# Kernel optimization log

Hardware: AMD Instinct MI355X
Metric: run time of the kernel (lower is better)

The kernel has to match this reference:

```python
import jax, jax.numpy as jnp
import numpy as np

B, S, D_MODEL, D_FF, E, K = 4, 2048, 1024, 4096, 8, 2
CAP_FACTOR = 1.0


def setup_inputs() -> dict:
    key = jax.random.key(0)
    ks = jax.random.split(key, 6)
    std = 0.02
    return {
        "x": jax.random.normal(ks[0], (B, S, D_MODEL), jnp.float32),
        "router_w": jax.random.normal(ks[1], (E, D_MODEL), jnp.float32) * std,  # Linear(d_model,E,bias=False) weight
        "w1": jax.random.normal(ks[2], (E, D_MODEL, D_FF), jnp.float32) * std,
        "b1": jnp.zeros((E, D_FF), jnp.float32),
        "w2": jax.random.normal(ks[3], (E, D_FF, D_MODEL), jnp.float32) * std,
        "b2": jnp.zeros((E, D_MODEL), jnp.float32),
    }


def reference(x, router_w, w1, b1, w2, b2):
    b, s, d = x.shape
    T = b * s
    e = router_w.shape[0]
    capacity = int(CAP_FACTOR * T / e)  # static
    xf = x.reshape(T, d)

    # --- routing ---
    logits = xf @ router_w.T                       # [T,E]
    probs = jax.nn.softmax(logits, axis=-1)
    vals, idx = jax.lax.top_k(probs, K)            # [T,K] values / expert ids
    vals = vals / vals.sum(-1, keepdims=True)

    # dense gate matrix [T,E]; top_k experts are distinct so this is a scatter of K weights per token
    ar = jnp.arange(T)
    gates = jnp.zeros((T, e), x.dtype).at[ar[:, None], idx].add(vals)

    # --- load-balancing loss ---
    counts = jnp.zeros((e,), jnp.float32).at[idx.reshape(-1)].add(1.0)
    ideal = T * K / e
    lb_loss = jnp.sum((counts - ideal) ** 2) / (T ** 2)

    # --- capacity-limited dispatch (first `capacity` tokens in token order per expert) ---
    mask = gates > 0                                               # [T,E]
    order = jnp.argsort(jnp.logical_not(mask), axis=0)[:capacity]  # stable: assigned tokens first, ascending token id -> [cap,E]
    valid = jnp.take_along_axis(mask, order, axis=0)               # [cap,E] token actually assigned & within capacity
    idx_ec = order.T                                               # [E,cap]

    # --- grouped expert MLP ---
    xg = xf[idx_ec]                                                # [E,cap,D]
    h = jax.nn.gelu(jnp.einsum('ecd,edf->ecf', xg, w1) + b1[:, None, :], approximate=False)
    y = jnp.einsum('ecf,efd->ecd', h, w2) + b2[:, None, :]         # [E,cap,D]

    # --- combine (scatter-add with routing weights; dropped/invalid slots get weight 0) ---
    wt = gates[idx_ec, jnp.arange(e)[:, None]] * valid.T           # [E,cap]
    out = jnp.zeros((T, d), x.dtype).at[idx_ec.reshape(-1)].add((y * wt[..., None]).reshape(-1, d))
    return out.reshape(b, s, d), lb_loss
```

## Files before the change

kernel.cpp:

```cpp
#include <hip/hip_runtime.h>
#include <hip/hip_bf16.h>

#define T_TOK 8192
#define DMODEL 1024
#define DFF 4096
#define NEXP 8
#define CAP 1024

typedef __attribute__((ext_vector_type(8))) __bf16 bf16x8;
typedef __attribute__((ext_vector_type(4))) float f32x4;

__device__ __forceinline__ unsigned short f2bf(float f) {
  union { float f; unsigned int u; } v;
  v.f = f;
  return (unsigned short)((v.u + 0x7fffu + ((v.u >> 16) & 1u)) >> 16);
}

__device__ __forceinline__ float bfbits2f(unsigned int lo16) {
  union { unsigned int u; float f; } v; v.u = lo16 << 16; return v.f;
}

__device__ __forceinline__ float fast_gelu(float v) {
  float x = fabsf(v) * 0.70710678118654752440f;
  float t = __builtin_amdgcn_rcpf(1.0f + 0.3275911f * x);
  float poly = t * (0.254829592f + t * (-0.284496736f + t * (1.421413741f +
               t * (-1.453152027f + t * 1.061405429f))));
  float er = 1.0f - poly * __expf(-x * x);
  float s = (v >= 0.0f) ? er : -er;
  return 0.5f * v * (1.0f + s);
}

__device__ __forceinline__ void load_lds16(const unsigned short* g, unsigned short* l) {
  __builtin_amdgcn_global_load_lds((const __attribute__((address_space(1))) void*)g,
                                   (__attribute__((address_space(3))) void*)l,
                                   16, 0, 0);
}

__global__ void k_router(const float* __restrict__ x, const float* __restrict__ rw,
                         unsigned short* __restrict__ xb,
                         int* __restrict__ tk_idx, float* __restrict__ tk_w,
                         int* __restrict__ tinv) {
  if (threadIdx.x < 8) tinv[blockIdx.x * 8 + threadIdx.x] = -1;
  int wv = threadIdx.x >> 6, lane = threadIdx.x & 63;
  int t = blockIdx.x * 4 + wv;
  const float4* xr = (const float4*)(x + (size_t)t * DMODEL);
  uint2* xbw = (uint2*)(xb + (size_t)t * DMODEL);
  float acc[NEXP];
#pragma unroll
  for (int e = 0; e < NEXP; ++e) acc[e] = 0.f;
#pragma unroll
  for (int j = 0; j < DMODEL / 256; ++j) {
    float4 v = xr[j * 64 + lane];
#pragma unroll
    for (int e = 0; e < NEXP; ++e) {
      float4 w = ((const float4*)(rw + e * DMODEL))[j * 64 + lane];
      acc[e] += v.x * w.x + v.y * w.y + v.z * w.z + v.w * w.w;
    }
    uint2 p;
    p.x = (unsigned int)f2bf(v.x) | ((unsigned int)f2bf(v.y) << 16);
    p.y = (unsigned int)f2bf(v.z) | ((unsigned int)f2bf(v.w) << 16);
    xbw[j * 64 + lane] = p;
  }
#pragma unroll
  for (int e = 0; e < NEXP; ++e)
    for (int off = 32; off; off >>= 1) acc[e] += __shfl_xor(acc[e], off);
  if (lane == 0) {
    int i0 = 0;
    for (int e = 1; e < NEXP; ++e) if (acc[e] > acc[i0]) i0 = e;
    int i1 = (i0 == 0) ? 1 : 0;
    for (int e = 0; e < NEXP; ++e) if (e != i0 && acc[e] > acc[i1]) i1 = e;
    float ex = expf(acc[i1] - acc[i0]);
    float w0 = 1.f / (1.f + ex);
    float w1 = ex / (1.f + ex);
    tk_idx[2 * t] = i0; tk_idx[2 * t + 1] = i1;
    tk_w[2 * t] = w0;  tk_w[2 * t + 1] = w1;
  }
}

__global__ void k_transpose_cvt(const float* __restrict__ src, unsigned short* __restrict__ dst,
                                int Kd, int Nd) {
  __shared__ unsigned short tile[64][73];
  int e = blockIdx.z;
  size_t k0 = (size_t)blockIdx.y * 64, n0 = (size_t)blockIdx.x * 64;
  int tid = threadIdx.x;
  const float* sb = src + (size_t)e * Kd * Nd;
  int r = tid >> 4, cg = (tid & 15) * 4;
  for (int rr = 0; rr < 4; ++rr) {
    int row = r + rr * 16;
    float4 v = *(const float4*)(sb + (k0 + row) * Nd + n0 + cg);
    tile[row][cg + 0] = f2bf(v.x);
    tile[row][cg + 1] = f2bf(v.y);
    tile[row][cg + 2] = f2bf(v.z);
    tile[row][cg + 3] = f2bf(v.w);
  }
  __syncthreads();
  unsigned short* db = dst + (size_t)e * Nd * Kd;
  int rn = tid >> 3, kg = (tid & 7) * 8;
  for (int rr = 0; rr < 2; ++rr) {
    int nrow = rn + rr * 32;
    union { unsigned short h[8]; uint4 v; } o;
#pragma unroll
    for (int j = 0; j < 8; ++j) o.h[j] = tile[kg + j][nrow];
    *(uint4*)(db + (n0 + nrow) * Kd + k0 + kg) = o.v;
  }
}

__global__ void k_scan(const int* __restrict__ tk_idx, const float* __restrict__ tk_w,
                       int* __restrict__ etok, float* __restrict__ egate,
                       int* __restrict__ tinv, int* __restrict__ counts) {
  __shared__ int wavecnt[8][16];
  __shared__ int waveoff[8][16];
  int e = blockIdx.x;
  int tid = threadIdx.x, lane = tid & 63, wv = tid >> 6;
  for (int i = tid; i < CAP; i += 1024) etok[e * CAP + i] = 0;
  unsigned long long lt = (1ULL << lane) - 1ULL;
  int pos[8], wh[8];
  bool mine[8];
#pragma unroll
  for (int c = 0; c < 8; ++c) {
    int t = c * 1024 + tid;
    int e0 = tk_idx[2 * t], e1 = tk_idx[2 * t + 1];
    bool is0 = (e0 == e), is1 = (e1 == e);
    mine[c] = is0 || is1;
    wh[c] = is1 ? 1 : 0;
    unsigned long long bal = __ballot(mine[c]);
    pos[c] = __popcll(bal & lt);
    if (lane == 0) wavecnt[c][wv] = __popcll(bal);
  }
  __syncthreads();
  if (tid == 0) {
    int s = 0;
    for (int c = 0; c < 8; ++c)
      for (int w = 0; w < 16; ++w) { waveoff[c][w] = s; s += wavecnt[c][w]; }
    counts[e] = s;
  }
  __syncthreads();
#pragma unroll
  for (int c = 0; c < 8; ++c) {
    if (mine[c]) {
      int t = c * 1024 + tid;
      int r = waveoff[c][wv] + pos[c];
      if (r < CAP) {
        etok[e * CAP + r] = t;
        egate[e * CAP + r] = tk_w[2 * t + wh[c]];
        tinv[2 * t + wh[c]] = e * CAP + r;
      }
    }
  }
}

__global__ __launch_bounds__(256) void k_gemm1(
    const unsigned short* __restrict__ xb, const unsigned short* __restrict__ w1t,
    const float* __restrict__ b1, const int* __restrict__ etok,
    unsigned short* __restrict__ H) {
  __shared__ __align__(16) unsigned short smem[24576];
  int tid = threadIdx.x;
  int lane = tid & 63, wv = tid >> 6;
  int bid = blockIdx.x;
  int e = bid >> 8;
  int b = bid & 255;
  int nl = b & 7, m = (b >> 3) & 7, nh = b >> 6;
  int m0 = m * 128, n0 = (nh * 8 + nl) * 128;

  const unsigned short* gA[2];
  const unsigned short* gB[2];
  int wb[2];
#pragma unroll
  for (int s = 0; s < 2; ++s) {
    int i = s * 256 + tid;
    int row = i >> 2;
    int q = (i & 3) ^ ((i >> 3) & 3);
    int tok = etok[e * CAP + m0 + row];
    gA[s] = xb + (size_t)tok * DMODEL + q * 8;
    gB[s] = w1t + ((size_t)e * DFF + n0 + row) * DMODEL + q * 8;
    wb[s] = (s * 256 + wv * 64) * 8;
  }

  f32x4 zero = {0.f, 0.f, 0.f, 0.f};
  f32x4 acc[4][4];
#pragma unroll
  for (int mi = 0; mi < 4; ++mi)
#pragma unroll
    for (int ni = 0; ni < 4; ++ni) acc[mi][ni] = zero;

  int wm = (wv >> 1) * 64, wn = (wv & 1) * 64;
  int fr = lane & 15, quad = lane >> 4;
  int cs = (quad ^ ((fr >> 1) & 3)) * 8;
  int aoff = (wm + fr) * 32 + cs;
  int boff = (wn + fr) * 32 + cs;

#pragma unroll
  for (int s = 0; s < 2; ++s) {
    load_lds16(gA[s], smem + wb[s]);
    load_lds16(gB[s], smem + 4096 + wb[s]);
  }
#pragma unroll
  for (int s = 0; s < 2; ++s) {
    load_lds16(gA[s] + 32, smem + 8192 + wb[s]);
    load_lds16(gB[s] + 32, smem + 8192 + 4096 + wb[s]);
  }

  const int NT = DMODEL / 32;
  int cur = 0, stg = 16384;
  for (int t = 0; t < NT; ++t) {
    if (t < NT - 1) asm volatile("s_waitcnt vmcnt(4)" ::: "memory");
    else            asm volatile("s_waitcnt vmcnt(0)" ::: "memory");
    __builtin_amdgcn_s_barrier();
    asm volatile("" ::: "memory");
    if (t + 2 < NT) {
      int kp = (t + 2) * 32;
#pragma unroll
      for (int s = 0; s < 2; ++s) {
        load_lds16(gA[s] + kp, smem + stg + wb[s]);
        load_lds16(gB[s] + kp, smem + stg + 4096 + wb[s]);
      }
      stg += 8192; if (stg == 24576) stg = 0;
    }
    const unsigned short* Ab = smem + cur;
    const unsigned short* Bb = Ab + 4096;
    bf16x8 av[4], bv[4];
#pragma unroll
    for (int mi = 0; mi < 4; ++mi) av[mi] = *(const bf16x8*)(Ab + aoff + mi * 512);
#pragma unroll
    for (int ni = 0; ni < 4; ++ni) bv[ni] = *(const bf16x8*)(Bb + boff + ni * 512);
#pragma unroll
    for (int mi = 0; mi < 4; ++mi)
#pragma unroll
      for (int ni = 0; ni < 4; ++ni)
        acc[mi][ni] = __builtin_amdgcn_mfma_f32_16x16x32_bf16(bv[ni], av[mi], acc[mi][ni], 0, 0, 0);
    cur += 8192; if (cur == 24576) cur = 0;
  }
  __syncthreads();

  unsigned short* EP = smem + wv * 1536;
#pragma unroll
  for (int ni = 0; ni < 4; ++ni) {
    float4 b4 = *(const float4*)(b1 + e * DFF + n0 + wn + ni * 16 + quad * 4);
#pragma unroll
    for (int mi = 0; mi < 4; ++mi) {
      float v0 = fast_gelu(acc[mi][ni][0] + b4.x);
      float v1 = fast_gelu(acc[mi][ni][1] + b4.y);
      float v2 = fast_gelu(acc[mi][ni][2] + b4.z);
      float v3 = fast_gelu(acc[mi][ni][3] + b4.w);
      uint2 p;
      p.x = (unsigned int)f2bf(v0) | ((unsigned int)f2bf(v1) << 16);
      p.y = (unsigned int)f2bf(v2) | ((unsigned int)f2bf(v3) << 16);
      *(uint2*)(EP + (mi * 16 + fr) * 24 + quad * 4) = p;
    }
#pragma unroll
    for (int t = 0; t < 2; ++t) {
      int row = t * 32 + (lane >> 1), chunk = lane & 1;
      uint4 v = *(const uint4*)(EP + row * 24 + chunk * 8);
      *(uint4*)(H + ((size_t)e * CAP + m0 + wm + row) * DFF + n0 + wn + ni * 16 + chunk * 8) = v;
    }
  }
}

__global__ __launch_bounds__(256) void k_gemm2(
    const unsigned short* __restrict__ H, const unsigned short* __restrict__ w2t,
    const float* __restrict__ b2, unsigned short* __restrict__ Y) {
  __shared__ __align__(16) unsigned short smem[24576];
  int tid = threadIdx.x;
  int lane = tid & 63, wv = tid >> 6;
  int bid = blockIdx.x;
  int e = bid & 7;
  int r = bid >> 3;
  int n0 = (r & 7) * 128;
  int m0 = (r >> 3) * 128;

  const unsigned short* gA[2];
  const unsigned short* gB[2];
  int wb[2];
#pragma unroll
  for (int s = 0; s < 2; ++s) {
    int i = s * 256 + tid;
    int row = i >> 2;
    int q = (i & 3) ^ ((i >> 3) & 3);
    gA[s] = H + ((size_t)e * CAP + m0 + row) * DFF + q * 8;
    gB[s] = w2t + ((size_t)e * DMODEL + n0 + row) * DFF + q * 8;
    wb[s] = (s * 256 + wv * 64) * 8;
  }

  f32x4 zero = {0.f, 0.f, 0.f, 0.f};
  f32x4 acc[4][4];
#pragma unroll
  for (int mi = 0; mi < 4; ++mi)
#pragma unroll
    for (int ni = 0; ni < 4; ++ni) acc[mi][ni] = zero;

  int wm = (wv >> 1) * 64, wn = (wv & 1) * 64;
  int fr = lane & 15, quad = lane >> 4;
  int cs = (quad ^ ((fr >> 1) & 3)) * 8;
  int aoff = (wm + fr) * 32 + cs;
  int boff = (wn + fr) * 32 + cs;

#pragma unroll
  for (int s = 0; s < 2; ++s) {
    load_lds16(gA[s], smem + wb[s]);
    load_lds16(gB[s], smem + 4096 + wb[s]);
  }
#pragma unroll
  for (int s = 0; s < 2; ++s) {
    load_lds16(gA[s] + 32, smem + 8192 + wb[s]);
    load_lds16(gB[s] + 32, smem + 8192 + 4096 + wb[s]);
  }

  const int NT = DFF / 32;
  int cur = 0, stg = 16384;
  for (int t = 0; t < NT; ++t) {
    if (t < NT - 1) asm volatile("s_waitcnt vmcnt(4)" ::: "memory");
    else            asm volatile("s_waitcnt vmcnt(0)" ::: "memory");
    __builtin_amdgcn_s_barrier();
    asm volatile("" ::: "memory");
    if (t + 2 < NT) {
      int kp = (t + 2) * 32;
#pragma unroll
      for (int s = 0; s < 2; ++s) {
        load_lds16(gA[s] + kp, smem + stg + wb[s]);
        load_lds16(gB[s] + kp, smem + stg + 4096 + wb[s]);
      }
      stg += 8192; if (stg == 24576) stg = 0;
    }
    const unsigned short* Ab = smem + cur;
    const unsigned short* Bb = Ab + 4096;
    bf16x8 av[4], bv[4];
#pragma unroll
    for (int mi = 0; mi < 4; ++mi) av[mi] = *(const bf16x8*)(Ab + aoff + mi * 512);
#pragma unroll
    for (int ni = 0; ni < 4; ++ni) bv[ni] = *(const bf16x8*)(Bb + boff + ni * 512);
#pragma unroll
    for (int mi = 0; mi < 4; ++mi)
#pragma unroll
      for (int ni = 0; ni < 4; ++ni)
        acc[mi][ni] = __builtin_amdgcn_mfma_f32_16x16x32_bf16(bv[ni], av[mi], acc[mi][ni], 0, 0, 0);
    cur += 8192; if (cur == 24576) cur = 0;
  }
  __syncthreads();

  unsigned short* EP = smem + wv * 1536;
#pragma unroll
  for (int ni = 0; ni < 4; ++ni) {
    float4 b4 = *(const float4*)(b2 + e * DMODEL + n0 + wn + ni * 16 + quad * 4);
#pragma unroll
    for (int mi = 0; mi < 4; ++mi) {
      uint2 p;
      p.x = (unsigned int)f2bf(acc[mi][ni][0] + b4.x) |
            ((unsigned int)f2bf(acc[mi][ni][1] + b4.y) << 16);
      p.y = (unsigned int)f2bf(acc[mi][ni][2] + b4.z) |
            ((unsigned int)f2bf(acc[mi][ni][3] + b4.w) << 16);
      *(uint2*)(EP + (mi * 16 + fr) * 24 + quad * 4) = p;
    }
#pragma unroll
    for (int t = 0; t < 2; ++t) {
      int row = t * 32 + (lane >> 1), chunk = lane & 1;
      uint4 v = *(const uint4*)(EP + row * 24 + chunk * 8);
      *(uint4*)(Y + ((size_t)e * CAP + m0 + wm + row) * DMODEL + n0 + wn + ni * 16 + chunk * 8) = v;
    }
  }
}

__global__ void k_combine(const unsigned short* __restrict__ Y,
                          const float* __restrict__ egate,
                          const int* __restrict__ tinv,
                          const int* __restrict__ counts,
                          float* __restrict__ out, float* __restrict__ loss_out) {
  int t = blockIdx.x, tid = threadIdx.x;
  int s0 = tinv[2 * t], s1 = tinv[2 * t + 1];
  int d0 = tid * 4;
  float a0 = 0.f, a1 = 0.f, a2 = 0.f, a3 = 0.f;
  if (s0 >= 0) {
    float g = egate[s0];
    uint2 v = *(const uint2*)(Y + (size_t)s0 * DMODEL + d0);
    a0 += g * bfbits2f(v.x & 0xffff); a1 += g * bfbits2f(v.x >> 16);
    a2 += g * bfbits2f(v.y & 0xffff); a3 += g * bfbits2f(v.y >> 16);
  }
  if (s1 >= 0) {
    float g = egate[s1];
    uint2 v = *(const uint2*)(Y + (size_t)s1 * DMODEL + d0);
    a0 += g * bfbits2f(v.x & 0xffff); a1 += g * bfbits2f(v.x >> 16);
    a2 += g * bfbits2f(v.y & 0xffff); a3 += g * bfbits2f(v.y >> 16);
  }
  float4 o = {a0, a1, a2, a3};
  *(float4*)(out + (size_t)t * DMODEL + d0) = o;
  if (t == 0 && tid == 0) {
    float loss = 0.f;
    for (int e = 0; e < NEXP; ++e) {
      float d = (float)counts[e] - 2048.0f;
      loss += d * d;
    }
    loss_out[0] = loss / (8192.0f * 8192.0f);
  }
}

extern "C" void kernel_launch(void* const* d_in, const int* in_sizes, int n_in,
                              void* d_out, int out_size, void* d_ws, size_t ws_size,
                              hipStream_t stream) {
  (void)in_sizes; (void)n_in; (void)ws_size; (void)out_size;
  const float* x  = (const float*)d_in[0];
  const float* rw = (const float*)d_in[1];
  const float* w1 = (const float*)d_in[2];
  const float* b1 = (const float*)d_in[3];
  const float* w2 = (const float*)d_in[4];
  const float* b2 = (const float*)d_in[5];
  float* out = (float*)d_out;

  char* ws = (char*)d_ws;
  const size_t XB_BYTES = (size_t)T_TOK * DMODEL * 2;
  const size_t WT_BYTES = (size_t)NEXP * DFF * DMODEL * 2;
  const size_t H_BYTES  = (size_t)NEXP * CAP * DFF * 2;
  unsigned short* xb = (unsigned short*)ws;
  unsigned short* Yb = xb;
  unsigned short* wT = (unsigned short*)(ws + XB_BYTES);
  unsigned short* Hb = (unsigned short*)(ws + XB_BYTES + WT_BYTES);
  char* small = ws + XB_BYTES + WT_BYTES + H_BYTES;
  int*   etok   = (int*)small;
  float* egate  = (float*)(small + NEXP * CAP * 4);
  int*   tkidx  = (int*)(small + 2 * NEXP * CAP * 4);
  float* tkw    = (float*)(small + 2 * NEXP * CAP * 4 + T_TOK * 2 * 4);
  int*   tinv   = (int*)(small + 2 * NEXP * CAP * 4 + 2 * T_TOK * 2 * 4);
  int*   counts = (int*)(small + 2 * NEXP * CAP * 4 + 3 * T_TOK * 2 * 4);

  k_router<<<T_TOK / 4, 256, 0, stream>>>(x, rw, xb, tkidx, tkw, tinv);
  k_scan<<<NEXP, 1024, 0, stream>>>(tkidx, tkw, etok, egate, tinv, counts);
  k_transpose_cvt<<<dim3(DFF / 64, DMODEL / 64, NEXP), 256, 0, stream>>>(w1, wT, DMODEL, DFF);
  k_gemm1<<<NEXP * 256, 256, 0, stream>>>(xb, wT, b1, etok, Hb);
  k_transpose_cvt<<<dim3(DMODEL / 64, DFF / 64, NEXP), 256, 0, stream>>>(w2, wT, DFF, DMODEL);
  k_gemm2<<<NEXP * 64, 256, 0, stream>>>(Hb, wT, b2, Yb);
  k_combine<<<T_TOK, 256, 0, stream>>>(Yb, egate, tinv, counts, out,
                                       out + (size_t)T_TOK * DMODEL);
}
```

Measured before the change: 544.7 us.

## Fuse combine into gemm2 epilogue with atomic scatter-add and smaller tiles

Removes the separate combine kernel and the bf16 Y buffer: gemm2 now applies bias and gate and atomically adds results directly into the fp32 output, which the router kernel zero-initialises. The gemm2 tile shrinks from 128x128 to 64x128 with double buffering instead of triple, doubling the block count so the grid fills more CUs. The atomics add contention and nondeterministic summation order, and the simpler pipeline with a full barrier per k-step may expose more memory latency.

```diff
diff --git a/kernel.cpp b/kernel.cpp
--- a/kernel.cpp
+++ b/kernel.cpp
@@ -14,10 +14,6 @@
   union { float f; unsigned int u; } v;
   v.f = f;
   return (unsigned short)((v.u + 0x7fffu + ((v.u >> 16) & 1u)) >> 16);
-}
-
-__device__ __forceinline__ float bfbits2f(unsigned int lo16) {
-  union { unsigned int u; float f; } v; v.u = lo16 << 16; return v.f;
 }
 
 __device__ __forceinline__ float fast_gelu(float v) {
@@ -39,10 +35,15 @@
 __global__ void k_router(const float* __restrict__ x, const float* __restrict__ rw,
                          unsigned short* __restrict__ xb,
                          int* __restrict__ tk_idx, float* __restrict__ tk_w,
-                         int* __restrict__ tinv) {
-  if (threadIdx.x < 8) tinv[blockIdx.x * 8 + threadIdx.x] = -1;
+                         float* __restrict__ out) {
   int wv = threadIdx.x >> 6, lane = threadIdx.x & 63;
   int t = blockIdx.x * 4 + wv;
+  {
+    float4 z = {0.f, 0.f, 0.f, 0.f};
+    float4* orow = (float4*)(out + (size_t)t * DMODEL);
+#pragma unroll
+    for (int j = 0; j < 4; ++j) orow[j * 64 + lane] = z;
+  }
   const float4* xr = (const float4*)(x + (size_t)t * DMODEL);
   uint2* xbw = (uint2*)(xb + (size_t)t * DMODEL);
   float acc[NEXP];
@@ -107,12 +108,15 @@
 
 __global__ void k_scan(const int* __restrict__ tk_idx, const float* __restrict__ tk_w,
                        int* __restrict__ etok, float* __restrict__ egate,
-                       int* __restrict__ tinv, int* __restrict__ counts) {
+                       int* __restrict__ counts) {
   __shared__ int wavecnt[8][16];
   __shared__ int waveoff[8][16];
   int e = blockIdx.x;
   int tid = threadIdx.x, lane = tid & 63, wv = tid >> 6;
-  for (int i = tid; i < CAP; i += 1024) etok[e * CAP + i] = 0;
+  for (int i = tid; i < CAP; i += 1024) {
+    etok[e * CAP + i] = 0;
+    egate[e * CAP + i] = 0.f;
+  }
   unsigned long long lt = (1ULL << lane) - 1ULL;
   int pos[8], wh[8];
   bool mine[8];
@@ -143,7 +147,6 @@
       if (r < CAP) {
         etok[e * CAP + r] = t;
         egate[e * CAP + r] = tk_w[2 * t + wh[c]];
-        tinv[2 * t + wh[c]] = e * CAP + r;
       }
     }
   }
@@ -258,137 +261,99 @@
 
 __global__ __launch_bounds__(256) void k_gemm2(
     const unsigned short* __restrict__ H, const unsigned short* __restrict__ w2t,
-    const float* __restrict__ b2, unsigned short* __restrict__ Y) {
-  __shared__ __align__(16) unsigned short smem[24576];
+    const float* __restrict__ b2, const int* __restrict__ etok,
+    const float* __restrict__ egate, const int* __restrict__ counts,
+    float* __restrict__ out, float* __restrict__ loss_out) {
+  __shared__ __align__(16) unsigned short smem[12288];
   int tid = threadIdx.x;
   int lane = tid & 63, wv = tid >> 6;
   int bid = blockIdx.x;
+  if (bid == 0 && tid == 0) {
+    float loss = 0.f;
+    for (int ee = 0; ee < NEXP; ++ee) {
+      float d = (float)counts[ee] - 2048.0f;
+      loss += d * d;
+    }
+    loss_out[0] = loss / (8192.0f * 8192.0f);
+  }
   int e = bid & 7;
   int r = bid >> 3;
   int n0 = (r & 7) * 128;
-  int m0 = (r >> 3) * 128;
-
-  const unsigned short* gA[2];
-  const unsigned short* gB[2];
-  int wb[2];
-#pragma unroll
-  for (int s = 0; s < 2; ++s) {
+  int m0 = (r >> 3) * 64;
+
+  const unsigned short* g[3];
+  int wb[3];
+#pragma unroll
+  for (int s = 0; s < 3; ++s) {
     int i = s * 256 + tid;
-    int row = i >> 2;
-    int q = (i & 3) ^ ((i >> 3) & 3);
-    gA[s] = H + ((size_t)e * CAP + m0 + row) * DFF + q * 8;
-    gB[s] = w2t + ((size_t)e * DMODEL + n0 + row) * DFF + q * 8;
-    wb[s] = (s * 256 + wv * 64) * 8;
+    wb[s] = i * 8;
+    if (s == 0) {
+      int row = i >> 2;
+      int q = (i & 3) ^ ((i >> 3) & 3);
+      g[s] = H + ((size_t)e * CAP + m0 + row) * DFF + q * 8;
+    } else {
+      int ii = i - 256;
+      int row = ii >> 2;
+      int q = (ii & 3) ^ ((ii >> 3) & 3);
+      g[s] = w2t + ((size_t)e * DMODEL + n0 + row) * DFF + q * 8;
+    }
   }
 
   f32x4 zero = {0.f, 0.f, 0.f, 0.f};
-  f32x4 acc[4][4];
+  f32x4 acc[4][2];
 #pragma unroll
   for (int mi = 0; mi < 4; ++mi)
 #pragma unroll
-    for (int ni = 0; ni < 4; ++ni) acc[mi][ni] = zero;
-
-  int wm = (wv >> 1) * 64, wn = (wv & 1) * 64;
+    for (int ni = 0; ni < 2; ++ni) acc[mi][ni] = zero;
+
+  int wn = wv * 32;
   int fr = lane & 15, quad = lane >> 4;
   int cs = (quad ^ ((fr >> 1) & 3)) * 8;
-  int aoff = (wm + fr) * 32 + cs;
+  int aoff = fr * 32 + cs;
   int boff = (wn + fr) * 32 + cs;
 
 #pragma unroll
-  for (int s = 0; s < 2; ++s) {
-    load_lds16(gA[s], smem + wb[s]);
-    load_lds16(gB[s], smem + 4096 + wb[s]);
-  }
-#pragma unroll
-  for (int s = 0; s < 2; ++s) {
-    load_lds16(gA[s] + 32, smem + 8192 + wb[s]);
-    load_lds16(gB[s] + 32, smem + 8192 + 4096 + wb[s]);
-  }
-
-  const int NT = DFF / 32;
-  int cur = 0, stg = 16384;
-  for (int t = 0; t < NT; ++t) {
-    if (t < NT - 1) asm volatile("s_waitcnt vmcnt(4)" ::: "memory");
-    else            asm volatile("s_waitcnt vmcnt(0)" ::: "memory");
-    __builtin_amdgcn_s_barrier();
-    asm volatile("" ::: "memory");
-    if (t + 2 < NT) {
-      int kp = (t + 2) * 32;
-#pragma unroll
-      for (int s = 0; s < 2; ++s) {
-        load_lds16(gA[s] + kp, smem + stg + wb[s]);
-        load_lds16(gB[s] + kp, smem + stg + 4096 + wb[s]);
+  for (int s = 0; s < 3; ++s) load_lds16(g[s], smem + wb[s]);
+  int buf = 0;
+  for (int k0 = 32; k0 <= DFF; k0 += 32) {
+    __syncthreads();
+    int nbuf = buf ^ 6144;
+    if (k0 < DFF) {
+#pragma unroll
+      for (int s = 0; s < 3; ++s) load_lds16(g[s] + k0, smem + nbuf + wb[s]);
+    }
+    const unsigned short* Ab = smem + buf;
+    const unsigned short* Bb = Ab + 2048;
+    bf16x8 av[4], bv[2];
+#pragma unroll
+    for (int mi = 0; mi < 4; ++mi) av[mi] = *(const bf16x8*)(Ab + aoff + mi * 512);
+#pragma unroll
+    for (int ni = 0; ni < 2; ++ni) bv[ni] = *(const bf16x8*)(Bb + boff + ni * 512);
+#pragma unroll
+    for (int mi = 0; mi < 4; ++mi)
+#pragma unroll
+      for (int ni = 0; ni < 2; ++ni)
+        acc[mi][ni] = __builtin_amdgcn_mfma_f32_16x16x32_bf16(bv[ni], av[mi], acc[mi][ni], 0, 0, 0);
+    buf = nbuf;
+  }
+
+  int slotbase = e * CAP + m0;
+#pragma unroll
+  for (int mi = 0; mi < 4; ++mi) {
+    int slot = slotbase + mi * 16 + fr;
+    float gate = egate[slot];
+    if (gate != 0.f) {
+      int tok = etok[slot];
+      float* orow = out + (size_t)tok * DMODEL + n0 + wn + quad * 4;
+#pragma unroll
+      for (int ni = 0; ni < 2; ++ni) {
+        float4 b4 = *(const float4*)(b2 + e * DMODEL + n0 + wn + ni * 16 + quad * 4);
+        atomicAdd(orow + ni * 16 + 0, gate * (acc[mi][ni][0] + b4.x));
+        atomicAdd(orow + ni * 16 + 1, gate * (acc[mi][ni][1] + b4.y));
+        atomicAdd(orow + ni * 16 + 2, gate * (acc[mi][ni][2] + b4.z));
+        atomicAdd(orow + ni * 16 + 3, gate * (acc[mi][ni][3] + b4.w));
       }
-      stg += 8192; if (stg == 24576) stg = 0;
-    }
-    const unsigned short* Ab = smem + cur;
-    const unsigned short* Bb = Ab + 4096;
-    bf16x8 av[4], bv[4];
-#pragma unroll
-    for (int mi = 0; mi < 4; ++mi) av[mi] = *(const bf16x8*)(Ab + aoff + mi * 512);
-#pragma unroll
-    for (int ni = 0; ni < 4; ++ni) bv[ni] = *(const bf16x8*)(Bb + boff + ni * 512);
-#pragma unroll
-    for (int mi = 0; mi < 4; ++mi)
-#pragma unroll
-      for (int ni = 0; ni < 4; ++ni)
-        acc[mi][ni] = __builtin_amdgcn_mfma_f32_16x16x32_bf16(bv[ni], av[mi], acc[mi][ni], 0, 0, 0);
-    cur += 8192; if (cur == 24576) cur = 0;
-  }
-  __syncthreads();
-
-  unsigned short* EP = smem + wv * 1536;
-#pragma unroll
-  for (int ni = 0; ni < 4; ++ni) {
-    float4 b4 = *(const float4*)(b2 + e * DMODEL + n0 + wn + ni * 16 + quad * 4);
-#pragma unroll
-    for (int mi = 0; mi < 4; ++mi) {
-      uint2 p;
-      p.x = (unsigned int)f2bf(acc[mi][ni][0] + b4.x) |
-            ((unsigned int)f2bf(acc[mi][ni][1] + b4.y) << 16);
-      p.y = (unsigned int)f2bf(acc[mi][ni][2] + b4.z) |
-            ((unsigned int)f2bf(acc[mi][ni][3] + b4.w) << 16);
-      *(uint2*)(EP + (mi * 16 + fr) * 24 + quad * 4) = p;
-    }
-#pragma unroll
-    for (int t = 0; t < 2; ++t) {
-      int row = t * 32 + (lane >> 1), chunk = lane & 1;
-      uint4 v = *(const uint4*)(EP + row * 24 + chunk * 8);
-      *(uint4*)(Y + ((size_t)e * CAP + m0 + wm + row) * DMODEL + n0 + wn + ni * 16 + chunk * 8) = v;
-    }
-  }
-}
-
-__global__ void k_combine(const unsigned short* __restrict__ Y,
-                          const float* __restrict__ egate,
-                          const int* __restrict__ tinv,
-                          const int* __restrict__ counts,
-                          float* __restrict__ out, float* __restrict__ loss_out) {
-  int t = blockIdx.x, tid = threadIdx.x;
-  int s0 = tinv[2 * t], s1 = tinv[2 * t + 1];
-  int d0 = tid * 4;
-  float a0 = 0.f, a1 = 0.f, a2 = 0.f, a3 = 0.f;
-  if (s0 >= 0) {
-    float g = egate[s0];
-    uint2 v = *(const uint2*)(Y + (size_t)s0 * DMODEL + d0);
-    a0 += g * bfbits2f(v.x & 0xffff); a1 += g * bfbits2f(v.x >> 16);
-    a2 += g * bfbits2f(v.y & 0xffff); a3 += g * bfbits2f(v.y >> 16);
-  }
-  if (s1 >= 0) {
-    float g = egate[s1];
-    uint2 v = *(const uint2*)(Y + (size_t)s1 * DMODEL + d0);
-    a0 += g * bfbits2f(v.x & 0xffff); a1 += g * bfbits2f(v.x >> 16);
-    a2 += g * bfbits2f(v.y & 0xffff); a3 += g * bfbits2f(v.y >> 16);
-  }
-  float4 o = {a0, a1, a2, a3};
-  *(float4*)(out + (size_t)t * DMODEL + d0) = o;
-  if (t == 0 && tid == 0) {
-    float loss = 0.f;
-    for (int e = 0; e < NEXP; ++e) {
-      float d = (float)counts[e] - 2048.0f;
-      loss += d * d;
-    }
-    loss_out[0] = loss / (8192.0f * 8192.0f);
+    }
   }
 }
 
@@ -409,7 +374,6 @@
   const size_t WT_BYTES = (size_t)NEXP * DFF * DMODEL * 2;
   const size_t H_BYTES  = (size_t)NEXP * CAP * DFF * 2;
   unsigned short* xb = (unsigned short*)ws;
-  unsigned short* Yb = xb;
   unsigned short* wT = (unsigned short*)(ws + XB_BYTES);
   unsigned short* Hb = (unsigned short*)(ws + XB_BYTES + WT_BYTES);
   char* small = ws + XB_BYTES + WT_BYTES + H_BYTES;
@@ -417,15 +381,13 @@
   float* egate  = (float*)(small + NEXP * CAP * 4);
   int*   tkidx  = (int*)(small + 2 * NEXP * CAP * 4);
   float* tkw    = (float*)(small + 2 * NEXP * CAP * 4 + T_TOK * 2 * 4);
-  int*   tinv   = (int*)(small + 2 * NEXP * CAP * 4 + 2 * T_TOK * 2 * 4);
-  int*   counts = (int*)(small + 2 * NEXP * CAP * 4 + 3 * T_TOK * 2 * 4);
-
-  k_router<<<T_TOK / 4, 256, 0, stream>>>(x, rw, xb, tkidx, tkw, tinv);
-  k_scan<<<NEXP, 1024, 0, stream>>>(tkidx, tkw, etok, egate, tinv, counts);
+  int*   counts = (int*)(small + 2 * NEXP * CAP * 4 + 2 * T_TOK * 2 * 4);
+
+  k_router<<<T_TOK / 4, 256, 0, stream>>>(x, rw, xb, tkidx, tkw, out);
+  k_scan<<<NEXP, 1024, 0, stream>>>(tkidx, tkw, etok, egate, counts);
   k_transpose_cvt<<<dim3(DFF / 64, DMODEL / 64, NEXP), 256, 0, stream>>>(w1, wT, DMODEL, DFF);
   k_gemm1<<<NEXP * 256, 256, 0, stream>>>(xb, wT, b1, etok, Hb);
   k_transpose_cvt<<<dim3(DMODEL / 64, DFF / 64, NEXP), 256, 0, stream>>>(w2, wT, DFF, DMODEL);
-  k_gemm2<<<NEXP * 64, 256, 0, stream>>>(Hb, wT, b2, Yb);
-  k_combine<<<T_TOK, 256, 0, stream>>>(Yb, egate, tinv, counts, out,
-                                       out + (size_t)T_TOK * DMODEL);
-}
+  k_gemm2<<<NEXP * 128, 256, 0, stream>>>(Hb, wT, b2, etok, egate, counts, out,
+                                          out + (size_t)T_TOK * DMODEL);
+}
```

After: 635.1 us. 16.6% more time.

## Merge router and both weight transposes into one prep kernel; double-buffer gemm2

Applied to the files above, without the earlier changes.

Folds the router and the w1/w2 bf16 transpose-convert kernels into a single block-role-dispatched launch, so all these memory-bound prep tasks share one grid. w2 gets its own workspace region when the workspace is large enough, otherwise it falls back to a separate transpose launch. gemm2 drops from a 3-stage to a 2-stage LDS pipeline with a full syncthreads every iteration. This cuts LDS use but exposes more load latency per k-step.

```diff
diff --git a/kernel.cpp b/kernel.cpp
--- a/kernel.cpp
+++ b/kernel.cpp
@@ -36,13 +36,13 @@
                                    16, 0, 0);
 }
 
-__global__ void k_router(const float* __restrict__ x, const float* __restrict__ rw,
-                         unsigned short* __restrict__ xb,
-                         int* __restrict__ tk_idx, float* __restrict__ tk_w,
-                         int* __restrict__ tinv) {
-  if (threadIdx.x < 8) tinv[blockIdx.x * 8 + threadIdx.x] = -1;
-  int wv = threadIdx.x >> 6, lane = threadIdx.x & 63;
-  int t = blockIdx.x * 4 + wv;
+__device__ __forceinline__ void router_role(
+    const float* __restrict__ x, const float* __restrict__ rw,
+    unsigned short* __restrict__ xb, int* __restrict__ tk_idx,
+    float* __restrict__ tk_w, int* __restrict__ tinv, int rbid, int tid) {
+  if (tid < 8) tinv[rbid * 8 + tid] = -1;
+  int wv = tid >> 6, lane = tid & 63;
+  int t = rbid * 4 + wv;
   const float4* xr = (const float4*)(x + (size_t)t * DMODEL);
   uint2* xbw = (uint2*)(xb + (size_t)t * DMODEL);
   float acc[NEXP];
@@ -77,12 +77,11 @@
   }
 }
 
-__global__ void k_transpose_cvt(const float* __restrict__ src, unsigned short* __restrict__ dst,
-                                int Kd, int Nd) {
+__device__ __forceinline__ void trans_role(
+    const float* __restrict__ src, unsigned short* __restrict__ dst,
+    int Kd, int Nd, int bx, int by, int e, int tid) {
   __shared__ unsigned short tile[64][73];
-  int e = blockIdx.z;
-  size_t k0 = (size_t)blockIdx.y * 64, n0 = (size_t)blockIdx.x * 64;
-  int tid = threadIdx.x;
+  size_t k0 = (size_t)by * 64, n0 = (size_t)bx * 64;
   const float* sb = src + (size_t)e * Kd * Nd;
   int r = tid >> 4, cg = (tid & 15) * 4;
   for (int rr = 0; rr < 4; ++rr) {
@@ -103,6 +102,28 @@
     for (int j = 0; j < 8; ++j) o.h[j] = tile[kg + j][nrow];
     *(uint4*)(db + (n0 + nrow) * Kd + k0 + kg) = o.v;
   }
+}
+
+__global__ __launch_bounds__(256) void k_prep(
+    const float* __restrict__ x, const float* __restrict__ rw,
+    unsigned short* __restrict__ xb, int* __restrict__ tkidx,
+    float* __restrict__ tkw, int* __restrict__ tinv,
+    const float* __restrict__ w1, unsigned short* __restrict__ w1t,
+    const float* __restrict__ w2, unsigned short* __restrict__ w2t) {
+  int bid = blockIdx.x, tid = threadIdx.x;
+  if (bid < 2048) { router_role(x, rw, xb, tkidx, tkw, tinv, bid, tid); return; }
+  bid -= 2048;
+  if (bid < 8192) {
+    trans_role(w1, w1t, DMODEL, DFF, bid & 63, (bid >> 6) & 15, bid >> 10, tid);
+    return;
+  }
+  bid -= 8192;
+  trans_role(w2, w2t, DFF, DMODEL, bid & 15, (bid >> 4) & 63, bid >> 10, tid);
+}
+
+__global__ __launch_bounds__(256) void k_transpose_cvt(
+    const float* __restrict__ src, unsigned short* __restrict__ dst, int Kd, int Nd) {
+  trans_role(src, dst, Kd, Nd, blockIdx.x, blockIdx.y, blockIdx.z, threadIdx.x);
 }
 
 __global__ void k_scan(const int* __restrict__ tk_idx, const float* __restrict__ tk_w,
@@ -259,7 +280,7 @@
 __global__ __launch_bounds__(256) void k_gemm2(
     const unsigned short* __restrict__ H, const unsigned short* __restrict__ w2t,
     const float* __restrict__ b2, unsigned short* __restrict__ Y) {
-  __shared__ __align__(16) unsigned short smem[24576];
+  __shared__ __align__(16) unsigned short smem[16384];
   int tid = threadIdx.x;
   int lane = tid & 63, wv = tid >> 6;
   int bid = blockIdx.x;
@@ -299,29 +320,18 @@
     load_lds16(gA[s], smem + wb[s]);
     load_lds16(gB[s], smem + 4096 + wb[s]);
   }
-#pragma unroll
-  for (int s = 0; s < 2; ++s) {
-    load_lds16(gA[s] + 32, smem + 8192 + wb[s]);
-    load_lds16(gB[s] + 32, smem + 8192 + 4096 + wb[s]);
-  }
-
-  const int NT = DFF / 32;
-  int cur = 0, stg = 16384;
-  for (int t = 0; t < NT; ++t) {
-    if (t < NT - 1) asm volatile("s_waitcnt vmcnt(4)" ::: "memory");
-    else            asm volatile("s_waitcnt vmcnt(0)" ::: "memory");
-    __builtin_amdgcn_s_barrier();
-    asm volatile("" ::: "memory");
-    if (t + 2 < NT) {
-      int kp = (t + 2) * 32;
+  int buf = 0;
+  for (int k0 = 32; k0 <= DFF; k0 += 32) {
+    __syncthreads();
+    int nbuf = buf ^ 8192;
+    if (k0 < DFF) {
 #pragma unroll
       for (int s = 0; s < 2; ++s) {
-        load_lds16(gA[s] + kp, smem + stg + wb[s]);
-        load_lds16(gB[s] + kp, smem + stg + 4096 + wb[s]);
+        load_lds16(gA[s] + k0, smem + nbuf + wb[s]);
+        load_lds16(gB[s] + k0, smem + nbuf + 4096 + wb[s]);
       }
-      stg += 8192; if (stg == 24576) stg = 0;
-    }
-    const unsigned short* Ab = smem + cur;
+    }
+    const unsigned short* Ab = smem + buf;
     const unsigned short* Bb = Ab + 4096;
     bf16x8 av[4], bv[4];
 #pragma unroll
@@ -333,7 +343,7 @@
 #pragma unroll
       for (int ni = 0; ni < 4; ++ni)
         acc[mi][ni] = __builtin_amdgcn_mfma_f32_16x16x32_bf16(bv[ni], av[mi], acc[mi][ni], 0, 0, 0);
-    cur += 8192; if (cur == 24576) cur = 0;
+    buf = nbuf;
   }
   __syncthreads();
 
@@ -395,7 +405,7 @@
 extern "C" void kernel_launch(void* const* d_in, const int* in_sizes, int n_in,
                               void* d_out, int out_size, void* d_ws, size_t ws_size,
                               hipStream_t stream) {
-  (void)in_sizes; (void)n_in; (void)ws_size; (void)out_size;
+  (void)in_sizes; (void)n_in; (void)out_size;
   const float* x  = (const float*)d_in[0];
   const float* rw = (const float*)d_in[1];
   const float* w1 = (const float*)d_in[2];
@@ -408,11 +418,17 @@
   const size_t XB_BYTES = (size_t)T_TOK * DMODEL * 2;
   const size_t WT_BYTES = (size_t)NEXP * DFF * DMODEL * 2;
   const size_t H_BYTES  = (size_t)NEXP * CAP * DFF * 2;
-  unsigned short* xb = (unsigned short*)ws;
-  unsigned short* Yb = xb;
-  unsigned short* wT = (unsigned short*)(ws + XB_BYTES);
-  unsigned short* Hb = (unsigned short*)(ws + XB_BYTES + WT_BYTES);
-  char* small = ws + XB_BYTES + WT_BYTES + H_BYTES;
+  const size_t SMALL_BYTES = 2 * NEXP * CAP * 4 + 3 * (size_t)T_TOK * 2 * 4 + 64;
+  const size_t NEED_FUSED = XB_BYTES + 2 * WT_BYTES + H_BYTES + SMALL_BYTES;
+  int fused = (ws_size >= NEED_FUSED);
+
+  unsigned short* xb  = (unsigned short*)ws;
+  unsigned short* Yb  = xb;
+  unsigned short* w1t = (unsigned short*)(ws + XB_BYTES);
+  unsigned short* w2t = fused ? (unsigned short*)(ws + XB_BYTES + WT_BYTES) : w1t;
+  char* after_wt = ws + XB_BYTES + (fused ? 2 : 1) * WT_BYTES;
+  unsigned short* Hb = (unsigned short*)after_wt;
+  char* small = after_wt + H_BYTES;
   int*   etok   = (int*)small;
   float* egate  = (float*)(small + NEXP * CAP * 4);
   int*   tkidx  = (int*)(small + 2 * NEXP * CAP * 4);
@@ -420,12 +436,14 @@
   int*   tinv   = (int*)(small + 2 * NEXP * CAP * 4 + 2 * T_TOK * 2 * 4);
   int*   counts = (int*)(small + 2 * NEXP * CAP * 4 + 3 * T_TOK * 2 * 4);
 
-  k_router<<<T_TOK / 4, 256, 0, stream>>>(x, rw, xb, tkidx, tkw, tinv);
+  int prep_blocks = 2048 + 8192 + (fused ? 8192 : 0);
+  k_prep<<<prep_blocks, 256, 0, stream>>>(x, rw, xb, tkidx, tkw, tinv, w1, w1t, w2, w2t);
   k_scan<<<NEXP, 1024, 0, stream>>>(tkidx, tkw, etok, egate, tinv, counts);
-  k_transpose_cvt<<<dim3(DFF / 64, DMODEL / 64, NEXP), 256, 0, stream>>>(w1, wT, DMODEL, DFF);
-  k_gemm1<<<NEXP * 256, 256, 0, stream>>>(xb, wT, b1, etok, Hb);
-  k_transpose_cvt<<<dim3(DMODEL / 64, DFF / 64, NEXP), 256, 0, stream>>>(w2, wT, DFF, DMODEL);
-  k_gemm2<<<NEXP * 64, 256, 0, stream>>>(Hb, wT, b2, Yb);
+  k_gemm1<<<NEXP * 256, 256, 0, stream>>>(xb, w1t, b1, etok, Hb);
+  if (!fused) {
+    k_transpose_cvt<<<dim3(DMODEL / 64, DFF / 64, NEXP), 256, 0, stream>>>(w2, w2t, DFF, DMODEL);
+  }
+  k_gemm2<<<NEXP * 64, 256, 0, stream>>>(Hb, w2t, b2, Yb);
   k_combine<<<T_TOK, 256, 0, stream>>>(Yb, egate, tinv, counts, out,
                                        out + (size_t)T_TOK * DMODEL);
 }
```

Result: no change. 535.1 us (-1.8%).
